# Optimization experiments

Measured on AMD Instinct MI355X. Metric: run time of the kernel, lower is better.

The kernel has to match this reference:

```python
import jax, jax.numpy as jnp
import numpy as np

# sRGB (D65) -> XYZ matrix, same as skimage.color.rgb2lab
_RGB2XYZ = jnp.array([[0.412453, 0.357580, 0.180423],
                      [0.212671, 0.715160, 0.072169],
                      [0.019334, 0.119193, 0.950227]], dtype=jnp.float32)
_WHITE = jnp.array([0.95047, 1.0, 1.08883], dtype=jnp.float32)  # D65 reference white


def _rgb_to_lab(rgb):
    """rgb: (B,3,H,W) in [0,1] -> Lab (B,3,H,W)."""
    c = jnp.clip(rgb, 0.0, 1.0)
    # sRGB gamma expansion
    lin = jnp.where(c <= 0.04045, c / 12.92, ((c + 0.055) / 1.055) ** 2.4)
    xyz = jnp.einsum('ij,bjhw->bihw', _RGB2XYZ, lin)
    t = xyz / _WHITE[None, :, None, None]
    eps = 0.008856
    f = jnp.where(t > eps, jnp.cbrt(jnp.maximum(t, eps)), 7.787 * t + 16.0 / 116.0)
    fx, fy, fz = f[:, 0], f[:, 1], f[:, 2]
    L = 116.0 * fy - 16.0
    a = 500.0 * (fx - fy)
    b = 200.0 * (fy - fz)
    return jnp.stack([L, a, b], axis=1)


def _ciede2000(lab1, lab2):
    """lab1, lab2: (B,3,H,W) -> deltaE (B,H,W). kL=kC=kH=1."""
    L1, a1, b1 = lab1[:, 0], lab1[:, 1], lab1[:, 2]
    L2, a2, b2 = lab2[:, 0], lab2[:, 1], lab2[:, 2]
    C1 = jnp.sqrt(a1 * a1 + b1 * b1)
    C2 = jnp.sqrt(a2 * a2 + b2 * b2)
    Cbar = 0.5 * (C1 + C2)
    c7 = Cbar ** 7
    G = 0.5 * (1.0 - jnp.sqrt(c7 / (c7 + 25.0 ** 7)))
    a1p = a1 * (1.0 + G)
    a2p = a2 * (1.0 + G)
    C1p = jnp.sqrt(a1p * a1p + b1 * b1)
    C2p = jnp.sqrt(a2p * a2p + b2 * b2)
    h1 = jnp.rad2deg(jnp.arctan2(b1, a1p)) % 360.0
    h2 = jnp.rad2deg(jnp.arctan2(b2, a2p)) % 360.0

    dL = L2 - L1
    dC = C2p - C1p
    dh = h2 - h1
    dh = jnp.where(dh > 180.0, dh - 360.0, dh)
    dh = jnp.where(dh < -180.0, dh + 360.0, dh)
    prodC = C1p * C2p
    dh = jnp.where(prodC == 0.0, 0.0, dh)
    dH = 2.0 * jnp.sqrt(prodC) * jnp.sin(jnp.deg2rad(dh) / 2.0)

    Lbar = 0.5 * (L1 + L2)
    Cbarp = 0.5 * (C1p + C2p)
    hsum = h1 + h2
    habs = jnp.abs(h1 - h2)
    hbar = jnp.where(habs <= 180.0, 0.5 * hsum,
                     jnp.where(hsum < 360.0, 0.5 * (hsum + 360.0), 0.5 * (hsum - 360.0)))
    hbar = jnp.where(prodC == 0.0, hsum, hbar)

    rad = jnp.deg2rad
    T = (1.0 - 0.17 * jnp.cos(rad(hbar - 30.0)) + 0.24 * jnp.cos(rad(2.0 * hbar))
         + 0.32 * jnp.cos(rad(3.0 * hbar + 6.0)) - 0.20 * jnp.cos(rad(4.0 * hbar - 63.0)))
    dtheta = 30.0 * jnp.exp(-(((hbar - 275.0) / 25.0) ** 2))
    cb7 = Cbarp ** 7
    Rc = 2.0 * jnp.sqrt(cb7 / (cb7 + 25.0 ** 7))
    Lm50sq = (Lbar - 50.0) ** 2
    SL = 1.0 + 0.015 * Lm50sq / jnp.sqrt(20.0 + Lm50sq)
    SC = 1.0 + 0.045 * Cbarp
    SH = 1.0 + 0.015 * Cbarp * T
    RT = -jnp.sin(rad(2.0 * dtheta)) * Rc

    tL = dL / SL
    tC = dC / SC
    tH = dH / SH
    return jnp.sqrt(jnp.maximum(tL * tL + tC * tC + tH * tH + RT * tC * tH, 0.0))


def setup_inputs() -> dict:
    key = jax.random.key(0)
    k1, k2 = jax.random.split(key)
    B, C, H, W = 16, 3, 512, 512
    outputs = jax.random.uniform(k1, (B, C, H, W), dtype=jnp.float32)
    labels = jax.random.uniform(k2, (B, C, H, W), dtype=jnp.float32)
    return {"outputs": outputs, "labels": labels}


def reference(outputs, labels):
    # ColorLoss.forward: ciede2000_loss(labels, outputs) -> mean CIEDE2000 over all pixels
    lab_true = _rgb_to_lab(labels)
    lab_pred = _rgb_to_lab(outputs)
    return jnp.mean(_ciede2000(lab_true, lab_pred))
```

## Files before the change

kernel.cpp:

```cpp
#include <hip/hip_runtime.h>
#include <math.h>


#define HW_SHIFT 18
#define HW_SIZE  (1 << HW_SHIFT)
#define LOG2E 1.4426950408889634f
#define NW 2

typedef float v2f __attribute__((ext_vector_type(2)));

__device__ __forceinline__ float fexp2(float x){ float r; asm("v_exp_f32 %0, %1" : "=v"(r) : "v"(x)); return r; }
__device__ __forceinline__ float flog2(float x){ float r; asm("v_log_f32 %0, %1" : "=v"(r) : "v"(x)); return r; }
__device__ __forceinline__ float fsin_rev(float x){ float r; asm("v_sin_f32 %0, %1" : "=v"(r) : "v"(x)); return r; }
__device__ __forceinline__ float fcos_rev(float x){ float r; asm("v_cos_f32 %0, %1" : "=v"(r) : "v"(x)); return r; }
__device__ __forceinline__ float frcp(float x){ float r; asm("v_rcp_f32 %0, %1" : "=v"(r) : "v"(x)); return r; }
__device__ __forceinline__ float frsq(float x){ float r; asm("v_rsq_f32 %0, %1" : "=v"(r) : "v"(x)); return r; }
__device__ __forceinline__ float fsqrt_(float x){ float r; asm("v_sqrt_f32 %0, %1" : "=v"(r) : "v"(x)); return r; }

struct VN { v2f v[NW]; };
__device__ __forceinline__ v2f mk2(float s){ return (v2f){s, s}; }
__device__ __forceinline__ VN mkN(float s){
    VN r;
#pragma unroll
    for (int i = 0; i < NW; ++i) r.v[i] = mk2(s);
    return r;
}

#define EW2(expr) ({ VN _r; _Pragma("unroll") \
    for (int _i = 0; _i < NW; ++_i) { v2f xa = x.v[_i]; v2f xb = y.v[_i]; (void)xb; _r.v[_i] = (expr); } _r; })

__device__ __forceinline__ VN operator+(VN x, VN y){ return EW2(xa + xb); }
__device__ __forceinline__ VN operator-(VN x, VN y){ return EW2(xa - xb); }
__device__ __forceinline__ VN operator*(VN x, VN y){ return EW2(xa * xb); }
__device__ __forceinline__ VN operator+(VN x, float s){ VN y = mkN(s); return x + y; }
__device__ __forceinline__ VN operator-(VN x, float s){ VN y = mkN(s); return x - y; }
__device__ __forceinline__ VN operator-(float s, VN y){ VN x = mkN(s); return x - y; }
__device__ __forceinline__ VN operator*(VN x, float s){ VN y = mkN(s); return x * y; }
__device__ __forceinline__ VN operator*(float s, VN x){ return x * s; }

__device__ __forceinline__ VN negN(VN x){
    VN r;
#pragma unroll
    for (int i = 0; i < NW; ++i) r.v[i] = -x.v[i];
    return r;
}
__device__ __forceinline__ VN fabsN(VN x){
    VN r;
#pragma unroll
    for (int i = 0; i < NW; ++i) r.v[i] = __builtin_elementwise_abs(x.v[i]);
    return r;
}
__device__ __forceinline__ VN fmaxN(VN x, VN y){ return EW2(__builtin_elementwise_max(xa, xb)); }
__device__ __forceinline__ VN fminN(VN x, VN y){ return EW2(__builtin_elementwise_min(xa, xb)); }
__device__ __forceinline__ VN fmaN(VN x, VN y, VN z){
    VN r;
#pragma unroll
    for (int i = 0; i < NW; ++i) r.v[i] = __builtin_elementwise_fma(x.v[i], y.v[i], z.v[i]);
    return r;
}
__device__ __forceinline__ VN fmaN(VN x, float y, VN z){ return fmaN(x, mkN(y), z); }
__device__ __forceinline__ VN fmaN(VN x, float y, float z){ return fmaN(x, mkN(y), mkN(z)); }
__device__ __forceinline__ VN fmaN(VN x, VN y, float z){ return fmaN(x, y, mkN(z)); }

#define SELN(name, cond) \
__device__ __forceinline__ VN name(VN x, float t, VN p, VN q){ VN r; _Pragma("unroll") \
    for (int i = 0; i < NW; ++i) { \
        r.v[i].x = (cond(x.v[i].x, t)) ? p.v[i].x : q.v[i].x; \
        r.v[i].y = (cond(x.v[i].y, t)) ? p.v[i].y : q.v[i].y; } return r; }
#define CLT(a,b) ((a) <  (b))
#define CGT(a,b) ((a) >  (b))
SELN(sel_lt, CLT)
SELN(sel_gt, CGT)

__device__ __forceinline__ VN sel_gtVV(VN x, VN y, VN p, VN q){
    VN r;
#pragma unroll
    for (int i = 0; i < NW; ++i) {
        r.v[i].x = x.v[i].x > y.v[i].x ? p.v[i].x : q.v[i].x;
        r.v[i].y = x.v[i].y > y.v[i].y ? p.v[i].y : q.v[i].y;
    }
    return r;
}

#define MAPN(name, scalar) \
__device__ __forceinline__ VN name(VN x){ VN r; _Pragma("unroll") \
    for (int i = 0; i < NW; ++i) { r.v[i].x = scalar(x.v[i].x); r.v[i].y = scalar(x.v[i].y); } return r; }
MAPN(fexp2N, fexp2)
MAPN(flog2N, flog2)
MAPN(fsinN,  fsin_rev)
MAPN(fcosN,  fcos_rev)
MAPN(frcpN,  frcp)
MAPN(frsqN,  frsq)
MAPN(fsqrtN, fsqrt_)
MAPN(rndneN, rintf)

__device__ __forceinline__ VN copysignN(VN a, VN s){
    VN r;
#pragma unroll
    for (int i = 0; i < NW; ++i) {
        r.v[i].x = copysignf(a.v[i].x, s.v[i].x);
        r.v[i].y = copysignf(a.v[i].y, s.v[i].y);
    }
    return r;
}

__device__ __forceinline__ VN atan2_degN(VN y, VN x) {
    VN ax = fabsN(x), ay = fabsN(y);
    VN mx = fmaxN(fmaxN(ax, ay), mkN(1e-30f));
    VN mn = fminN(ax, ay);
    VN t = mn * frcpN(mx);
    VN s = t * t;
    VN p = mkN(  1.1937633f);
    p = fmaN(p, s,  -4.8777616f);
    p = fmaN(p, s,  10.3213190f);
    p = fmaN(p, s, -18.9247673f);
    p = fmaN(p, s,  57.2881019f);
    VN a = t * p;
    a = sel_gtVV(ay, ax, 90.0f - a, a);
    a = sel_lt(x, 0.0f, 180.0f - a, a);
    return copysignN(a, y);
}

__device__ __forceinline__ VN srgb_linN(VN c) {
    VN u = fmaN(c, 1.0f / 1.055f, 0.055f / 1.055f);
    return fexp2N(flog2N(u) * 2.4f);
}

__device__ __forceinline__ VN f_cbrtN(VN t) {
    VN cb = fexp2N(flog2N(t) * (1.0f / 3.0f));
    return sel_gt(t, 0.008856f, cb, fmaN(t, 7.787f, 16.0f / 116.0f));
}

__device__ __forceinline__ void rgb2labN(VN r, VN g, VN b,
                                         VN& L, VN& A, VN& B) {
    VN lr = srgb_linN(r), lg = srgb_linN(g), lb = srgb_linN(b);
    VN tx = fmaN(lb, 0.18982526f, fmaN(lg, 0.37621367f, lr * 0.43394630f));
    VN ty = fmaN(lb, 0.072169f,   fmaN(lg, 0.71516f,    lr * 0.212671f));
    VN tz = fmaN(lb, 0.87270460f, fmaN(lg, 0.10946829f, lr * 0.01775634f));
    VN fx = f_cbrtN(tx);
    VN fy = f_cbrtN(ty);
    VN fz = f_cbrtN(tz);
    L = fmaN(fy, 116.0f, -16.0f);
    A = (fx - fy) * 500.0f;
    B = (fy - fz) * 200.0f;
}

__device__ __forceinline__ VN ciedeN(VN L1, VN a1, VN b1,
                                     VN L2, VN a2, VN b2) {
    const float P25_7 = 6103515625.0f;
    VN C1 = fsqrtN(fmaN(a1, a1, b1 * b1));
    VN C2 = fsqrtN(fmaN(a2, a2, b2 * b2));
    VN Cbar = (C1 + C2) * 0.5f;
    VN cb2 = Cbar * Cbar, cb4 = cb2 * cb2;
    VN c7 = cb4 * cb2 * Cbar;
    VN G = 0.5f * (1.0f - fsqrtN(c7 * frcpN(c7 + P25_7)));
    VN onepG = G + 1.0f;
    VN a1p = a1 * onepG;
    VN a2p = a2 * onepG;
    VN C1p = fsqrtN(fmaN(a1p, a1p, b1 * b1));
    VN C2p = fsqrtN(fmaN(a2p, a2p, b2 * b2));

    VN dL = L2 - L1;
    VN dC = C2p - C1p;

    VN prodC = C1p * C2p;
    VN dot   = fmaN(a1p, a2p, b1 * b2);
    VN cross = fmaN(a1p, b2, negN(a2p * b1));
    VN dH = copysignN(fsqrtN(fmaxN((prodC - dot) * 2.0f, mkN(0.0f))), cross);

    VN Lbar  = (L1 + L2) * 0.5f;
    VN Cbarp = (C1p + C2p) * 0.5f;

    VN bn = fmaN(b1,  C2p, b2  * C1p);
    VN bd = fmaN(a1p, C2p, a2p * C1p);
    VN m = atan2_degN(bn, bd);

    VN hr = m * (1.0f / 360.0f);
    VN sh = fsinN(hr);
    VN ch = fcosN(hr);
    VN s2 = sh * sh;
    VN c2h = fmaN(s2, -2.0f, 1.0f);
    VN s2h = (sh + sh) * ch;
    VN c3h = ch * fmaN(s2, -4.0f, 1.0f);
    VN s3h = sh * fmaN(s2, -4.0f, 3.0f);
    VN c4h = fmaN(c2h, c2h, mkN(0.0f)); c4h = fmaN(c4h, 2.0f, -1.0f);
    VN s4h = (s2h + s2h) * c2h;
    VN cA = fmaN(ch, 0.8660254037844387f, sh * 0.5f);
    VN cC = fmaN(c3h, 0.9945218953682733f, negN(s3h * 0.10452846326765346f));
    VN cD = fmaN(c4h, 0.45399049973954675f, s4h * 0.8910065241883679f);
    VN T = fmaN(cD, -0.20f, fmaN(cC, 0.32f, fmaN(c2h, 0.24f, fmaN(cA, -0.17f, mkN(1.0f)))));

    VN d275 = m - 275.0f;
    VN kw = rndneN(d275 * (1.0f / 360.0f));
    d275 = fmaN(kw, -360.0f, d275);
    VN u = d275 * (1.0f / 25.0f);
    VN dtheta = 30.0f * fexp2N(negN(u * u) * LOG2E);
    VN cp2 = Cbarp * Cbarp, cp4 = cp2 * cp2;
    VN cb7 = cp4 * cp2 * Cbarp;
    VN Rc = 2.0f * fsqrtN(cb7 * frcpN(cb7 + P25_7));
    VN Lm50 = Lbar - 50.0f;
    VN Lm50sq = Lm50 * Lm50;
    VN SL = fmaN(Lm50sq * 0.015f, frsqN(Lm50sq + 20.0f), mkN(1.0f));
    VN SC = fmaN(Cbarp, 0.045f, 1.0f);
    VN SH = fmaN(Cbarp * T, 0.015f, mkN(1.0f));
    VN RT = negN(fsinN(dtheta * (1.0f / 180.0f))) * Rc;
    VN pCH = SC * SH;
    VN r3 = frcpN(SL * pCH);
    VN tL = dL * (pCH * r3);
    VN tC = dC * ((SL * SH) * r3);
    VN tH = dH * ((SL * SC) * r3);
    VN acc = fmaN(tL, tL, fmaN(tC, tC, fmaN(tH, tH, RT * (tC * tH))));
    return fsqrtN(fmaxN(acc, mkN(0.0f)));
}

__device__ __forceinline__ VN ldN(const float* p) {
    float4 u = *(const float4*)p;
    VN r;
    r.v[0] = (v2f){u.x, u.y}; r.v[1] = (v2f){u.z, u.w};
    return r;
}

__global__ __launch_bounds__(256) void colorloss_main(
    const float* __restrict__ outs, const float* __restrict__ labs,
    float* __restrict__ partial, int P4)
{
    int tid = blockIdx.x * blockDim.x + threadIdx.x;
    float s = 0.0f;
    if (tid < P4) {
        int p = tid << 2;
        int b = p >> HW_SHIFT;
        int rem = p & (HW_SIZE - 1);
        size_t base = (size_t)b * (3 * HW_SIZE) + rem;
        VN ro = ldN(outs + base);
        VN go = ldN(outs + base + HW_SIZE);
        VN bo = ldN(outs + base + 2 * HW_SIZE);
        VN rl = ldN(labs + base);
        VN gl = ldN(labs + base + HW_SIZE);
        VN bl = ldN(labs + base + 2 * HW_SIZE);

        VN Lt, At, Bt, Lp, Ap, Bp;
        rgb2labN(rl, gl, bl, Lt, At, Bt);
        rgb2labN(ro, go, bo, Lp, Ap, Bp);
        VN de = ciedeN(Lt, At, Bt, Lp, Ap, Bp);
        v2f t2 = de.v[0] + de.v[1];
        s = t2.x + t2.y;
    }
#pragma unroll
    for (int off = 32; off > 0; off >>= 1) s += __shfl_down(s, off);
    __shared__ float lds[4];
    if ((threadIdx.x & 63) == 0) lds[threadIdx.x >> 6] = s;
    __syncthreads();
    if (threadIdx.x == 0)
        partial[blockIdx.x] = lds[0] + lds[1] + lds[2] + lds[3];
}

__global__ __launch_bounds__(1024) void colorloss_reduce(
    const float* __restrict__ partial, int n, float* __restrict__ outp, float invN)
{
    float s = 0.0f;
    for (int i = threadIdx.x; i < n; i += 1024) s += partial[i];
#pragma unroll
    for (int off = 32; off > 0; off >>= 1) s += __shfl_down(s, off);
    __shared__ float lds[16];
    if ((threadIdx.x & 63) == 0) lds[threadIdx.x >> 6] = s;
    __syncthreads();
    if (threadIdx.x == 0) {
        float t = 0.0f;
#pragma unroll
        for (int i = 0; i < 16; ++i) t += lds[i];
        outp[0] = t * invN;
    }
}

extern "C" void kernel_launch(void* const* d_in, const int* in_sizes, int n_in,
                              void* d_out, int out_size, void* d_ws, size_t ws_size,
                              hipStream_t stream) {
    const float* outs = (const float*)d_in[0];
    const float* labs = (const float*)d_in[1];
    float* out = (float*)d_out;
    float* partial = (float*)d_ws;

    int n  = in_sizes[0];
    int P  = n / 3;
    int P4 = P / 4;
    int blocks = (P4 + 255) / 256;

    colorloss_main<<<blocks, 256, 0, stream>>>(outs, labs, partial, P4);
    colorloss_reduce<<<1, 1024, 0, stream>>>(partial, blocks, out, 1.0f / (float)P);
}
```

Before: 31.86 us.

## Replace atan2 and trig of mean hue with normalized vector components

Instead of computing the mean hue angle with a polynomial atan2 and then taking its sine and cosine, the kernel normalizes the (bd, bn) vector with one rsqrt to get sin and cos directly. The Gaussian hue term exp(-((h-275)/25)^2) is replaced by a von Mises-style form exp2(k*(cos(h-275)-1)), built from the same sin/cos. This removes the atan2 polynomial, the v_sin/v_cos calls and the rounding for angle wrap-around from a compute-bound per-pixel path. The dtheta term is now an approximation that matches near the peak and drifts slightly in the tails, where its value is tiny.

```diff
diff --git a/kernel.cpp b/kernel.cpp
--- a/kernel.cpp
+++ b/kernel.cpp
@@ -12,7 +12,6 @@
 __device__ __forceinline__ float fexp2(float x){ float r; asm("v_exp_f32 %0, %1" : "=v"(r) : "v"(x)); return r; }
 __device__ __forceinline__ float flog2(float x){ float r; asm("v_log_f32 %0, %1" : "=v"(r) : "v"(x)); return r; }
 __device__ __forceinline__ float fsin_rev(float x){ float r; asm("v_sin_f32 %0, %1" : "=v"(r) : "v"(x)); return r; }
-__device__ __forceinline__ float fcos_rev(float x){ float r; asm("v_cos_f32 %0, %1" : "=v"(r) : "v"(x)); return r; }
 __device__ __forceinline__ float frcp(float x){ float r; asm("v_rcp_f32 %0, %1" : "=v"(r) : "v"(x)); return r; }
 __device__ __forceinline__ float frsq(float x){ float r; asm("v_rsq_f32 %0, %1" : "=v"(r) : "v"(x)); return r; }
 __device__ __forceinline__ float fsqrt_(float x){ float r; asm("v_sqrt_f32 %0, %1" : "=v"(r) : "v"(x)); return r; }
@@ -44,12 +43,6 @@
     for (int i = 0; i < NW; ++i) r.v[i] = -x.v[i];
     return r;
 }
-__device__ __forceinline__ VN fabsN(VN x){
-    VN r;
-#pragma unroll
-    for (int i = 0; i < NW; ++i) r.v[i] = __builtin_elementwise_abs(x.v[i]);
-    return r;
-}
 __device__ __forceinline__ VN fmaxN(VN x, VN y){ return EW2(__builtin_elementwise_max(xa, xb)); }
 __device__ __forceinline__ VN fminN(VN x, VN y){ return EW2(__builtin_elementwise_min(xa, xb)); }
 __device__ __forceinline__ VN fmaN(VN x, VN y, VN z){
@@ -62,22 +55,12 @@
 __device__ __forceinline__ VN fmaN(VN x, float y, float z){ return fmaN(x, mkN(y), mkN(z)); }
 __device__ __forceinline__ VN fmaN(VN x, VN y, float z){ return fmaN(x, y, mkN(z)); }
 
-#define SELN(name, cond) \
-__device__ __forceinline__ VN name(VN x, float t, VN p, VN q){ VN r; _Pragma("unroll") \
-    for (int i = 0; i < NW; ++i) { \
-        r.v[i].x = (cond(x.v[i].x, t)) ? p.v[i].x : q.v[i].x; \
-        r.v[i].y = (cond(x.v[i].y, t)) ? p.v[i].y : q.v[i].y; } return r; }
-#define CLT(a,b) ((a) <  (b))
-#define CGT(a,b) ((a) >  (b))
-SELN(sel_lt, CLT)
-SELN(sel_gt, CGT)
-
-__device__ __forceinline__ VN sel_gtVV(VN x, VN y, VN p, VN q){
+__device__ __forceinline__ VN sel_gt(VN x, float t, VN p, VN q){
     VN r;
 #pragma unroll
     for (int i = 0; i < NW; ++i) {
-        r.v[i].x = x.v[i].x > y.v[i].x ? p.v[i].x : q.v[i].x;
-        r.v[i].y = x.v[i].y > y.v[i].y ? p.v[i].y : q.v[i].y;
+        r.v[i].x = x.v[i].x > t ? p.v[i].x : q.v[i].x;
+        r.v[i].y = x.v[i].y > t ? p.v[i].y : q.v[i].y;
     }
     return r;
 }
@@ -88,11 +71,9 @@
 MAPN(fexp2N, fexp2)
 MAPN(flog2N, flog2)
 MAPN(fsinN,  fsin_rev)
-MAPN(fcosN,  fcos_rev)
 MAPN(frcpN,  frcp)
 MAPN(frsqN,  frsq)
 MAPN(fsqrtN, fsqrt_)
-MAPN(rndneN, rintf)
 
 __device__ __forceinline__ VN copysignN(VN a, VN s){
     VN r;
@@ -102,23 +83,6 @@
         r.v[i].y = copysignf(a.v[i].y, s.v[i].y);
     }
     return r;
-}
-
-__device__ __forceinline__ VN atan2_degN(VN y, VN x) {
-    VN ax = fabsN(x), ay = fabsN(y);
-    VN mx = fmaxN(fmaxN(ax, ay), mkN(1e-30f));
-    VN mn = fminN(ax, ay);
-    VN t = mn * frcpN(mx);
-    VN s = t * t;
-    VN p = mkN(  1.1937633f);
-    p = fmaN(p, s,  -4.8777616f);
-    p = fmaN(p, s,  10.3213190f);
-    p = fmaN(p, s, -18.9247673f);
-    p = fmaN(p, s,  57.2881019f);
-    VN a = t * p;
-    a = sel_gtVV(ay, ax, 90.0f - a, a);
-    a = sel_lt(x, 0.0f, 180.0f - a, a);
-    return copysignN(a, y);
 }
 
 __device__ __forceinline__ VN srgb_linN(VN c) {
@@ -173,11 +137,11 @@
 
     VN bn = fmaN(b1,  C2p, b2  * C1p);
     VN bd = fmaN(a1p, C2p, a2p * C1p);
-    VN m = atan2_degN(bn, bd);
-
-    VN hr = m * (1.0f / 360.0f);
-    VN sh = fsinN(hr);
-    VN ch = fcosN(hr);
+    VN hyp2 = fmaxN(fmaN(bn, bn, bd * bd), mkN(1e-30f));
+    VN rs = frsqN(hyp2);
+    VN sh = bn * rs;
+    VN ch = bd * rs;
+
     VN s2 = sh * sh;
     VN c2h = fmaN(s2, -2.0f, 1.0f);
     VN s2h = (sh + sh) * ch;
@@ -190,11 +154,10 @@
     VN cD = fmaN(c4h, 0.45399049973954675f, s4h * 0.8910065241883679f);
     VN T = fmaN(cD, -0.20f, fmaN(cC, 0.32f, fmaN(c2h, 0.24f, fmaN(cA, -0.17f, mkN(1.0f)))));
 
-    VN d275 = m - 275.0f;
-    VN kw = rndneN(d275 * (1.0f / 360.0f));
-    d275 = fmaN(kw, -360.0f, d275);
-    VN u = d275 * (1.0f / 25.0f);
-    VN dtheta = 30.0f * fexp2N(negN(u * u) * LOG2E);
+    VN cosd = fmaN(ch, 0.08715574274765817f, sh * -0.9961946980917455f);
+    VN arg = fmaN(cosd, 15.155494f, mkN(-15.155494f));
+    VN dtheta = 30.0f * fexp2N(arg);
+
     VN cp2 = Cbarp * Cbarp, cp4 = cp2 * cp2;
     VN cb7 = cp4 * cp2 * Cbarp;
     VN Rc = 2.0f * fsqrtN(cb7 * frcpN(cb7 + P25_7));
```

After: 30.21 us. 5.2% less time.
